# Optimization experiments

Measured on AMD Instinct MI355X. Metric: run time of the kernel, lower is better.

## Reference

```python
import jax, jax.numpy as jnp
import numpy as np

B, S, D, H, E, K = 4, 512, 512, 2048, 8, 2
LN_EPS = 1e-5

def _ln(x, g, b):
    m = jnp.mean(x, axis=-1, keepdims=True)
    v = jnp.var(x, axis=-1, keepdims=True)
    return (x - m) / jnp.sqrt(v + LN_EPS) * g + b

def setup_inputs() -> dict:
    key = jax.random.key(0)
    ks = jax.random.split(key, 8)
    s = 0.02
    return {
        "x": jax.random.normal(ks[0], (B, S, D), dtype=jnp.float32),
        "context": jax.random.normal(ks[1], (B, S, D), dtype=jnp.float32),
        "quality": jax.random.uniform(ks[2], (B, 1), dtype=jnp.float32),
        "rn_g": jnp.ones((D,), jnp.float32), "rn_b": jnp.zeros((D,), jnp.float32),
        "cn_g": jnp.ones((D,), jnp.float32), "cn_b": jnp.zeros((D,), jnp.float32),
        "ctx_W": jax.random.normal(ks[3], (D, D), dtype=jnp.float32) * s,
        "ctx_b": jnp.zeros((D,), jnp.float32),
        "qual_W": jax.random.normal(ks[4], (1, D), dtype=jnp.float32) * s,
        "qual_b": jnp.zeros((D,), jnp.float32),
        "rtr_W": jax.random.normal(ks[5], (D, E), dtype=jnp.float32) * s,
        "rtr_b": jnp.zeros((E,), jnp.float32),
        "temperature": jnp.asarray(1.0, jnp.float32),
        "W1": jax.random.normal(ks[6], (E, D, H), dtype=jnp.float32) * s,
        "b1": jnp.zeros((E, H), jnp.float32),
        "W2": jax.random.normal(ks[7], (E, H, D), dtype=jnp.float32) * s,
        "b2": jnp.zeros((E, D), jnp.float32),
    }

def reference(x, context, quality, rn_g, rn_b, cn_g, cn_b, ctx_W, ctx_b,
              qual_W, qual_b, rtr_W, rtr_b, temperature, W1, b1, W2, b2):
    # router features: LN(x) + context_proj(LN(context)) + quality_proj(quality)
    rf = _ln(x, rn_g, rn_b) + (_ln(context, cn_g, cn_b) @ ctx_W + ctx_b)
    q = quality[:, None, :]                      # [B,1,1]
    rf = rf + (q @ qual_W + qual_b)              # broadcast [B,1,D] over seq
    logits = (rf @ rtr_W + rtr_b) / jnp.maximum(temperature, 0.25)  # [B,S,E]
    # eval mode: no router noise, no dropout
    topk_logits, topk_idx = jax.lax.top_k(logits, K)
    gates = jax.nn.softmax(topk_logits, axis=-1)                    # [B,S,K]
    # per-token per-expert combine weight (equivalent to masked dispatch)
    combine = jnp.sum(gates[..., None] * jax.nn.one_hot(topk_idx, E, dtype=x.dtype), axis=-2)  # [B,S,E]
    # dense all-expert FFN, combined with (mostly zero) gate weights
    h = jax.nn.gelu(jnp.einsum('bsd,edh->bseh', x, W1) + b1, approximate=False)  # [B,S,E,H]
    y = jnp.einsum('bseh,ehd->bsed', h, W2) + b2                                 # [B,S,E,D]
    out = jnp.einsum('bsed,bse->bsd', y, combine)
    # aux losses
    probs = jax.nn.softmax(logits, axis=-1)
    importance = probs.mean(axis=(0, 1))
    load_balance = jnp.mean((importance - 1.0 / E) ** 2)
    router_z = jnp.mean(jax.scipy.special.logsumexp(logits, axis=-1) ** 2)
    entropy = jnp.mean(-jnp.sum(probs * jnp.log(jnp.clip(probs, 1e-9, None)), axis=-1))
    aux = load_balance + 1e-3 * router_z - 1e-3 * entropy
    return out, load_balance, router_z, entropy, aux
```

## Files before the change

kernel.cpp:

```cpp
#include <hip/hip_runtime.h>
#include <hip/hip_bf16.h>
#include <math.h>

#define Bb 4
#define Ss 512
#define Dd 512
#define Hh 2048
#define Ee 8
#define TOKENS 2048
#define CAP 2048

typedef __attribute__((ext_vector_type(8))) _Float16 f16x8;
typedef __attribute__((ext_vector_type(4))) _Float16 f16x4;
typedef __attribute__((ext_vector_type(4))) float f32x4;

#define WS_CNT   0
#define WS_OFFS  32
#define WS_M1    128
#define WS_QV    16512
#define WS_CB    16544
#define WS_LIST  16640
#define WS_GLIST 82176
#define WS_LOG   147712
#define WS_XF    (WS_LOG + 65536)
#define WS_W1F   (WS_XF + 2097152)
#define WS_W2F   (WS_W1F + 16777216)
#define WS_HF    (WS_W2F + 16777216)

__device__ __forceinline__ float wred(float v) {
#pragma unroll
  for (int o = 32; o > 0; o >>= 1) v += __shfl_down(v, o);
  return v;
}

__device__ __forceinline__ float wredx(float v) {
#pragma unroll
  for (int o = 32; o > 0; o >>= 1) v += __shfl_xor(v, o);
  return v;
}

__device__ __forceinline__ float block_sum(float v, float* s4, int tid) {
  v = wred(v);
  __syncthreads();
  if ((tid & 63) == 0) s4[tid >> 6] = v;
  __syncthreads();
  return s4[0] + s4[1] + s4[2] + s4[3];
}

__device__ __forceinline__ float gelu_f(float v) {
  return 0.5f * v * (1.0f + erff(v * 0.7071067811865475f));
}

#define GL16(gp, lp) __builtin_amdgcn_global_load_lds( \
    (const __attribute__((address_space(1))) void*)(gp), \
    (__attribute__((address_space(3))) void*)(lp), 16, 0, 0)

__global__ __launch_bounds__(64) void k_precomp(
    const float* __restrict__ ctx_W, const float* __restrict__ rtr_W,
    const float* __restrict__ rtr_b, const float* __restrict__ qual_W,
    const float* __restrict__ qual_b, const float* __restrict__ ctx_b,
    float* __restrict__ M1, float* __restrict__ qv, float* __restrict__ cb) {
  int d = blockIdx.x;
  int lane = threadIdx.x;
  if (d < Dd) {
    float acc[Ee] = {0.f, 0.f, 0.f, 0.f, 0.f, 0.f, 0.f, 0.f};
    for (int k = lane; k < Dd; k += 64) {
      float cw = ctx_W[d * Dd + k];
      const float* r = rtr_W + k * Ee;
#pragma unroll
      for (int e = 0; e < Ee; e++) acc[e] += cw * r[e];
    }
#pragma unroll
    for (int e = 0; e < Ee; e++) acc[e] = wred(acc[e]);
    if (lane == 0) {
#pragma unroll
      for (int e = 0; e < Ee; e++) M1[d * Ee + e] = acc[e];
    }
  } else {
    float aq[Ee] = {0.f, 0.f, 0.f, 0.f, 0.f, 0.f, 0.f, 0.f};
    float ab[Ee] = {0.f, 0.f, 0.f, 0.f, 0.f, 0.f, 0.f, 0.f};
    for (int k = lane; k < Dd; k += 64) {
      float qw = qual_W[k];
      float bb = ctx_b[k] + qual_b[k];
      const float* r = rtr_W + k * Ee;
#pragma unroll
      for (int e = 0; e < Ee; e++) {
        aq[e] += qw * r[e];
        ab[e] += bb * r[e];
      }
    }
#pragma unroll
    for (int e = 0; e < Ee; e++) {
      aq[e] = wred(aq[e]);
      ab[e] = wred(ab[e]);
    }
    if (lane == 0) {
#pragma unroll
      for (int e = 0; e < Ee; e++) {
        qv[e] = aq[e];
        cb[e] = ab[e] + rtr_b[e];
      }
    }
  }
}

__global__ __launch_bounds__(256) void k_logits(
    const float* __restrict__ x, const float* __restrict__ ctx,
    const float* __restrict__ quality, const float* __restrict__ rn_g,
    const float* __restrict__ rn_b, const float* __restrict__ cn_g,
    const float* __restrict__ cn_b, const float* __restrict__ rtr_W,
    const float* __restrict__ M1, const float* __restrict__ qv,
    const float* __restrict__ cb, const float* __restrict__ temperature,
    float* __restrict__ logitsS, _Float16* __restrict__ xf) {
  int wid = threadIdx.x >> 6, lane = threadIdx.x & 63;
  int t = blockIdx.x * 4 + wid;
  int d0 = lane * 8;

  float xv[8], cv[8];
  *(float4*)&xv[0] = *(const float4*)(x + (size_t)t * Dd + d0);
  *(float4*)&xv[4] = *(const float4*)(x + (size_t)t * Dd + d0 + 4);
  *(float4*)&cv[0] = *(const float4*)(ctx + (size_t)t * Dd + d0);
  *(float4*)&cv[4] = *(const float4*)(ctx + (size_t)t * Dd + d0 + 4);

  f16x8 xh;
#pragma unroll
  for (int d = 0; d < 8; d++) xh[d] = (_Float16)xv[d];
  *(f16x8*)(xf + (size_t)t * Dd + d0) = xh;

  float sx = 0.f, sc = 0.f;
#pragma unroll
  for (int d = 0; d < 8; d++) { sx += xv[d]; sc += cv[d]; }
  float mx = wredx(sx) * (1.f / Dd);
  float mc = wredx(sc) * (1.f / Dd);
  float vx = 0.f, vc = 0.f;
#pragma unroll
  for (int d = 0; d < 8; d++) {
    vx += (xv[d] - mx) * (xv[d] - mx);
    vc += (cv[d] - mc) * (cv[d] - mc);
  }
  float rsx = rsqrtf(wredx(vx) * (1.f / Dd) + 1e-5f);
  float rsc = rsqrtf(wredx(vc) * (1.f / Dd) + 1e-5f);

  float rg[8], rb[8], cg[8], cbb[8];
  *(float4*)&rg[0] = *(const float4*)(rn_g + d0);
  *(float4*)&rg[4] = *(const float4*)(rn_g + d0 + 4);
  *(float4*)&rb[0] = *(const float4*)(rn_b + d0);
  *(float4*)&rb[4] = *(const float4*)(rn_b + d0 + 4);
  *(float4*)&cg[0] = *(const float4*)(cn_g + d0);
  *(float4*)&cg[4] = *(const float4*)(cn_g + d0 + 4);
  *(float4*)&cbb[0] = *(const float4*)(cn_b + d0);
  *(float4*)&cbb[4] = *(const float4*)(cn_b + d0 + 4);

  float lg[Ee] = {0.f, 0.f, 0.f, 0.f, 0.f, 0.f, 0.f, 0.f};
#pragma unroll
  for (int d = 0; d < 8; d++) {
    float xn = (xv[d] - mx) * rsx * rg[d] + rb[d];
    float cn = (cv[d] - mc) * rsc * cg[d] + cbb[d];
    float rw[8], m1[8];
    *(float4*)&rw[0] = *(const float4*)(rtr_W + (size_t)(d0 + d) * Ee);
    *(float4*)&rw[4] = *(const float4*)(rtr_W + (size_t)(d0 + d) * Ee + 4);
    *(float4*)&m1[0] = *(const float4*)(M1 + (size_t)(d0 + d) * Ee);
    *(float4*)&m1[4] = *(const float4*)(M1 + (size_t)(d0 + d) * Ee + 4);
#pragma unroll
    for (int e = 0; e < Ee; e++) lg[e] += xn * rw[e] + cn * m1[e];
  }
#pragma unroll
  for (int e = 0; e < Ee; e++) lg[e] = wredx(lg[e]);

  if (lane == 0) {
    float invT = 1.f / fmaxf(temperature[0], 0.25f);
    float q = quality[t / Ss];
    float L[8];
#pragma unroll
    for (int e = 0; e < Ee; e++) L[e] = (lg[e] + q * qv[e] + cb[e]) * invT;
    *(float4*)(logitsS + (size_t)t * Ee) = *(float4*)&L[0];
    *(float4*)(logitsS + (size_t)t * Ee + 4) = *(float4*)&L[4];
  }
}

__global__ __launch_bounds__(256) void k_select(
    const float* __restrict__ logitsS, int* __restrict__ cnt,
    int* __restrict__ offs, int* __restrict__ list,
    float* __restrict__ glist, float* __restrict__ out) {
  __shared__ int scnt[Ee];
  __shared__ float s4[4];
  int tid = threadIdx.x;
  if (tid < Ee) scnt[tid] = 0;
  __syncthreads();

  float impL[Ee] = {0.f, 0.f, 0.f, 0.f, 0.f, 0.f, 0.f, 0.f};
  float zL = 0.f, eL = 0.f;

#pragma unroll
  for (int j = 0; j < 8; j++) {
    int t = j * 256 + tid;
    float L[8];
    *(float4*)&L[0] = *(const float4*)(logitsS + (size_t)t * Ee);
    *(float4*)&L[4] = *(const float4*)(logitsS + (size_t)t * Ee + 4);

    int i0 = 0;
#pragma unroll
    for (int e = 1; e < Ee; e++)
      if (L[e] > L[i0]) i0 = e;
    int i1 = (i0 == 0) ? 1 : 0;
#pragma unroll
    for (int e = 0; e < Ee; e++)
      if (e != i0 && L[e] > L[i1]) i1 = e;

    float e1 = __expf(L[i1] - L[i0]);
    float g0 = 1.f / (1.f + e1);
    float g1 = e1 / (1.f + e1);

    float m = L[i0];
    float p[8];
    float sum = 0.f;
#pragma unroll
    for (int e = 0; e < Ee; e++) {
      p[e] = __expf(L[e] - m);
      sum += p[e];
    }
    float lse = m + __logf(sum);
    float inv = 1.f / sum;
    zL += lse * lse;
#pragma unroll
    for (int e = 0; e < Ee; e++) {
      p[e] *= inv;
      eL -= p[e] * __logf(fmaxf(p[e], 1e-9f));
      impL[e] += p[e];
    }

    int s0 = atomicAdd(&scnt[i0], 1);
    list[i0 * CAP + s0] = t;
    glist[i0 * CAP + s0] = g0;
    int s1 = atomicAdd(&scnt[i1], 1);
    list[i1 * CAP + s1] = t;
    glist[i1 * CAP + s1] = g1;
  }

  float impS[Ee];
#pragma unroll
  for (int e = 0; e < Ee; e++) impS[e] = block_sum(impL[e], s4, tid);
  float zS = block_sum(zL, s4, tid);
  float eS = block_sum(eL, s4, tid);
  __syncthreads();

  if (tid == 0) {
    int s = 0;
#pragma unroll
    for (int e = 0; e < Ee; e++) {
      cnt[e] = scnt[e];
      offs[e] = s;
      s += scnt[e];
    }
    float lb = 0.f;
#pragma unroll
    for (int e = 0; e < Ee; e++) {
      float v = impS[e] * (1.f / TOKENS) - (1.f / Ee);
      lb += v * v;
    }
    lb *= (1.f / Ee);
    float rz = zS * (1.f / TOKENS);
    float en = eS * (1.f / TOKENS);
    float* sp = out + (size_t)Bb * Ss * Dd;
    sp[0] = lb;
    sp[1] = rz;
    sp[2] = en;
    sp[3] = lb + 0.001f * rz - 0.001f * en;
  }
}

__device__ __forceinline__ void convT_tile(const float* __restrict__ src,
    _Float16* __restrict__ dst, int R, int C, int bx, float* ls) {
  int nr = R >> 6, ncc = C >> 6;
  int e = bx / (nr * ncc);
  int rem = bx % (nr * ncc);
  int rt = rem / ncc, ct = rem % ncc;
  int tid = threadIdx.x;
  const float* s0 = src + (size_t)e * R * C + (size_t)(rt * 64) * C + ct * 64;
#pragma unroll
  for (int j = 0; j < 4; j++) {
    int li = j * 256 + tid;
    int rr = li >> 4, c4 = (li & 15) << 2;
    float4 v = *(const float4*)(s0 + (size_t)rr * C + c4);
    ls[rr * 65 + c4] = v.x;
    ls[rr * 65 + c4 + 1] = v.y;
    ls[rr * 65 + c4 + 2] = v.z;
    ls[rr * 65 + c4 + 3] = v.w;
  }
  __syncthreads();
#pragma unroll
  for (int j = 0; j < 4; j++) {
    int li = j * 256 + tid;
    int on = li >> 4, k4 = (li & 15) << 2;
    f16x4 o;
    o[0] = (_Float16)ls[(k4 + 0) * 65 + on];
    o[1] = (_Float16)ls[(k4 + 1) * 65 + on];
    o[2] = (_Float16)ls[(k4 + 2) * 65 + on];
    o[3] = (_Float16)ls[(k4 + 3) * 65 + on];
    *(f16x4*)(dst + ((size_t)e * C + ct * 64 + on) * R + rt * 64 + k4) = o;
  }
}

__global__ __launch_bounds__(256) void k_convW(
    const float* __restrict__ W1, const float* __restrict__ W2,
    _Float16* __restrict__ w1f, _Float16* __restrict__ w2f) {
  __shared__ float ls[64 * 65];
  int bx = blockIdx.x;
  if (bx < Ee * 8 * 32) {
    convT_tile(W1, w1f, Dd, Hh, bx, ls);
  } else {
    convT_tile(W2, w2f, Hh, Dd, bx - Ee * 8 * 32, ls);
  }
}

__global__ __launch_bounds__(256) void k_mg1(
    const _Float16* __restrict__ xf, const _Float16* __restrict__ w1f,
    const float* __restrict__ b1,
    const int* __restrict__ cnt, const int* __restrict__ offs,
    const int* __restrict__ list, _Float16* __restrict__ hf) {
  int bx = blockIdx.x;
  int e = bx >> 9;
  int r = (bx >> 4) & 31;
  int c = bx & 15;
  int ne = cnt[e];
  if (r * 64 >= ne) return;
  int off = offs[e];

  __shared__ _Float16 As[2][4 * 64 * 8];
  __shared__ _Float16 Bs[2][4 * 128 * 8];
  __shared__ int stok[64];

  int tid = threadIdx.x;
  if (tid < 64) {
    int row = r * 64 + tid;
    stok[tid] = list[e * CAP + ((row < ne) ? row : (ne - 1))];
  }
  __syncthreads();

  int ag = tid >> 6, arow = tid & 63;
  size_t asrc = (size_t)stok[arow] * Dd + ag * 8;
  int bg0 = tid >> 7, brow0 = tid & 127;
  size_t bsrc0 = ((size_t)(e * Hh + c * 128 + brow0)) * Dd + bg0 * 8;
  size_t bsrc1 = bsrc0 + 16;
  int aL = (ag * 64 + arow) * 8;
  int bL0 = (bg0 * 128 + brow0) * 8;
  int bL1 = ((bg0 + 2) * 128 + brow0) * 8;

  int lane = tid & 63, wid = tid >> 6;
  int wm = wid >> 1, wn = wid & 1;
  int l15 = lane & 15, lg = lane >> 4;

  f32x4 acc[2][4] = {};

  GL16(xf + asrc, &As[0][aL]);
  GL16(w1f + bsrc0, &Bs[0][bL0]);
  GL16(w1f + bsrc1, &Bs[0][bL1]);
  __syncthreads();

  int cur = 0;
  for (int k0 = 32; k0 <= Dd; k0 += 32) {
    if (k0 < Dd) {
      GL16(xf + asrc + k0, &As[cur ^ 1][aL]);
      GL16(w1f + bsrc0 + k0, &Bs[cur ^ 1][bL0]);
      GL16(w1f + bsrc1 + k0, &Bs[cur ^ 1][bL1]);
    }
    f16x8 a[2], b[4];
#pragma unroll
    for (int m = 0; m < 2; m++)
      a[m] = *(const f16x8*)&As[cur][(lg * 64 + wm * 32 + m * 16 + l15) * 8];
#pragma unroll
    for (int n = 0; n < 4; n++)
      b[n] = *(const f16x8*)&Bs[cur][(lg * 128 + wn * 64 + n * 16 + l15) * 8];
#pragma unroll
    for (int m = 0; m < 2; m++)
#pragma unroll
      for (int n = 0; n < 4; n++)
        acc[m][n] = __builtin_amdgcn_mfma_f32_16x16x32_f16(a[m], b[n], acc[m][n], 0, 0, 0);
    __syncthreads();
    cur ^= 1;
  }

  int lg4 = lg * 4;
#pragma unroll
  for (int n = 0; n < 4; n++) {
    int colg = c * 128 + wn * 64 + n * 16 + l15;
    float bias = b1[e * Hh + colg];
#pragma unroll
    for (int m = 0; m < 2; m++) {
#pragma unroll
      for (int j = 0; j < 4; j++) {
        int rowl = r * 64 + wm * 32 + m * 16 + lg4 + j;
        if (rowl < ne)
          hf[(size_t)(off + rowl) * Hh + colg] = (_Float16)gelu_f(acc[m][n][j] + bias);
      }
    }
  }
}

__global__ __launch_bounds__(256) void k_mg2(
    const _Float16* __restrict__ hf, const _Float16* __restrict__ w2f,
    const float* __restrict__ b2,
    const int* __restrict__ cnt, const int* __restrict__ offs,
    const int* __restrict__ list, const float* __restrict__ glist,
    float* __restrict__ out) {
  int bx = blockIdx.x;
  int e = bx >> 8;
  int r = (bx >> 3) & 31;
  int c = (bx >> 1) & 3;
  int kS = bx & 1;
  int ne = cnt[e];
  if (r * 64 >= ne) return;
  int off = offs[e];

  __shared__ _Float16 As[2][4 * 64 * 8];
  __shared__ _Float16 Bs[2][4 * 128 * 8];

  int tid = threadIdx.x;
  int ag = tid >> 6, arow = tid & 63;
  int ar = r * 64 + arow;
  if (ar >= ne) ar = ne - 1;
  size_t kb = (size_t)kS * 1024;
  size_t asrc = (size_t)(off + ar) * Hh + kb + ag * 8;
  int bg0 = tid >> 7, brow0 = tid & 127;
  size_t bsrc0 = ((size_t)(e * Dd + c * 128 + brow0)) * Hh + kb + bg0 * 8;
  size_t bsrc1 = bsrc0 + 16;
  int aL = (ag * 64 + arow) * 8;
  int bL0 = (bg0 * 128 + brow0) * 8;
  int bL1 = ((bg0 + 2) * 128 + brow0) * 8;

  int lane = tid & 63, wid = tid >> 6;
  int wm = wid >> 1, wn = wid & 1;
  int l15 = lane & 15, lg = lane >> 4;

  f32x4 acc[2][4] = {};

  GL16(hf + asrc, &As[0][aL]);
  GL16(w2f + bsrc0, &Bs[0][bL0]);
  GL16(w2f + bsrc1, &Bs[0][bL1]);
  __syncthreads();

  int cur = 0;
  for (int k0 = 32; k0 <= 1024; k0 += 32) {
    if (k0 < 1024) {
      GL16(hf + asrc + k0, &As[cur ^ 1][aL]);
      GL16(w2f + bsrc0 + k0, &Bs[cur ^ 1][bL0]);
      GL16(w2f + bsrc1 + k0, &Bs[cur ^ 1][bL1]);
    }
    f16x8 a[2], b[4];
#pragma unroll
    for (int m = 0; m < 2; m++)
      a[m] = *(const f16x8*)&As[cur][(lg * 64 + wm * 32 + m * 16 + l15) * 8];
#pragma unroll
    for (int n = 0; n < 4; n++)
      b[n] = *(const f16x8*)&Bs[cur][(lg * 128 + wn * 64 + n * 16 + l15) * 8];
#pragma unroll
    for (int m = 0; m < 2; m++)
#pragma unroll
      for (int n = 0; n < 4; n++)
        acc[m][n] = __builtin_amdgcn_mfma_f32_16x16x32_f16(a[m], b[n], acc[m][n], 0, 0, 0);
    __syncthreads();
    cur ^= 1;
  }

  int lg4 = lg * 4;
#pragma unroll
  for (int m = 0; m < 2; m++) {
#pragma unroll
    for (int j = 0; j < 4; j++) {
      int rowl = r * 64 + wm * 32 + m * 16 + lg4 + j;
      if (rowl < ne) {
        int tok = list[e * CAP + rowl];
        float gte = glist[e * CAP + rowl];
#pragma unroll
        for (int n = 0; n < 4; n++) {
          int colg = c * 128 + wn * 64 + n * 16 + l15;
          float v = acc[m][n][j] + (kS == 0 ? b2[e * Dd + colg] : 0.f);
          atomicAdd(&out[(size_t)tok * Dd + colg], gte * v);
        }
      }
    }
  }
}

extern "C" void kernel_launch(void* const* d_in, const int* in_sizes, int n_in,
                              void* d_out, int out_size, void* d_ws, size_t ws_size,
                              hipStream_t stream) {
  const float* x = (const float*)d_in[0];
  const float* ctx = (const float*)d_in[1];
  const float* quality = (const float*)d_in[2];
  const float* rn_g = (const float*)d_in[3];
  const float* rn_b = (const float*)d_in[4];
  const float* cn_g = (const float*)d_in[5];
  const float* cn_b = (const float*)d_in[6];
  const float* ctx_W = (const float*)d_in[7];
  const float* ctx_b = (const float*)d_in[8];
  const float* qual_W = (const float*)d_in[9];
  const float* qual_b = (const float*)d_in[10];
  const float* rtr_W = (const float*)d_in[11];
  const float* rtr_b = (const float*)d_in[12];
  const float* temperature = (const float*)d_in[13];
  const float* W1 = (const float*)d_in[14];
  const float* b1 = (const float*)d_in[15];
  const float* W2 = (const float*)d_in[16];
  const float* b2 = (const float*)d_in[17];
  float* out = (float*)d_out;

  char* w = (char*)d_ws;
  int* cnt = (int*)(w + WS_CNT);
  int* offs = (int*)(w + WS_OFFS);
  float* M1 = (float*)(w + WS_M1);
  float* qv = (float*)(w + WS_QV);
  float* cb = (float*)(w + WS_CB);
  int* list = (int*)(w + WS_LIST);
  float* glist = (float*)(w + WS_GLIST);
  float* logitsS = (float*)(w + WS_LOG);
  _Float16* xf = (_Float16*)(w + WS_XF);
  _Float16* w1f = (_Float16*)(w + WS_W1F);
  _Float16* w2f = (_Float16*)(w + WS_W2F);
  _Float16* hf = (_Float16*)(w + WS_HF);

  hipMemsetAsync(d_out, 0, (size_t)out_size * sizeof(float), stream);

  k_precomp<<<513, 64, 0, stream>>>(ctx_W, rtr_W, rtr_b, qual_W, qual_b, ctx_b, M1, qv, cb);
  k_logits<<<TOKENS / 4, 256, 0, stream>>>(x, ctx, quality, rn_g, rn_b, cn_g, cn_b, rtr_W,
                                           M1, qv, cb, temperature, logitsS, xf);
  k_convW<<<Ee * 8 * 32 * 2, 256, 0, stream>>>(W1, W2, w1f, w2f);
  k_select<<<1, 256, 0, stream>>>(logitsS, cnt, offs, list, glist, out);
  k_mg1<<<Ee * 32 * 16, 256, 0, stream>>>(xf, w1f, b1, cnt, offs, list, hf);
  k_mg2<<<Ee * 32 * 4 * 2, 256, 0, stream>>>(hf, w2f, b2, cnt, offs, list, glist, out);
}
```

Before: 297.7 us.

## Enlarge grouped GEMM tiles to 128x128, widen K step, fuse weight conversion launch

```diff
diff --git a/kernel.cpp b/kernel.cpp
--- a/kernel.cpp
+++ b/kernel.cpp
@@ -55,13 +55,57 @@
     (const __attribute__((address_space(1))) void*)(gp), \
     (__attribute__((address_space(3))) void*)(lp), 16, 0, 0)
 
-__global__ __launch_bounds__(64) void k_precomp(
+__device__ __forceinline__ void convT_tile(const float* __restrict__ src,
+    _Float16* __restrict__ dst, int R, int C, int bx, float* ls) {
+  int nr = R >> 6, ncc = C >> 6;
+  int e = bx / (nr * ncc);
+  int rem = bx % (nr * ncc);
+  int rt = rem / ncc, ct = rem % ncc;
+  int tid = threadIdx.x;
+  const float* s0 = src + (size_t)e * R * C + (size_t)(rt * 64) * C + ct * 64;
+#pragma unroll
+  for (int j = 0; j < 4; j++) {
+    int li = j * 256 + tid;
+    int rr = li >> 4, c4 = (li & 15) << 2;
+    float4 v = *(const float4*)(s0 + (size_t)rr * C + c4);
+    ls[rr * 65 + c4] = v.x;
+    ls[rr * 65 + c4 + 1] = v.y;
+    ls[rr * 65 + c4 + 2] = v.z;
+    ls[rr * 65 + c4 + 3] = v.w;
+  }
+  __syncthreads();
+#pragma unroll
+  for (int j = 0; j < 4; j++) {
+    int li = j * 256 + tid;
+    int on = li >> 4, k4 = (li & 15) << 2;
+    f16x4 o;
+    o[0] = (_Float16)ls[(k4 + 0) * 65 + on];
+    o[1] = (_Float16)ls[(k4 + 1) * 65 + on];
+    o[2] = (_Float16)ls[(k4 + 2) * 65 + on];
+    o[3] = (_Float16)ls[(k4 + 3) * 65 + on];
+    *(f16x4*)(dst + ((size_t)e * C + ct * 64 + on) * R + rt * 64 + k4) = o;
+  }
+}
+
+__global__ __launch_bounds__(256) void k_pre(
     const float* __restrict__ ctx_W, const float* __restrict__ rtr_W,
     const float* __restrict__ rtr_b, const float* __restrict__ qual_W,
     const float* __restrict__ qual_b, const float* __restrict__ ctx_b,
-    float* __restrict__ M1, float* __restrict__ qv, float* __restrict__ cb) {
-  int d = blockIdx.x;
-  int lane = threadIdx.x;
+    const float* __restrict__ W1, const float* __restrict__ W2,
+    float* __restrict__ M1, float* __restrict__ qv, float* __restrict__ cb,
+    _Float16* __restrict__ w1f, _Float16* __restrict__ w2f) {
+  __shared__ float ls[64 * 65];
+  int bx = blockIdx.x;
+  if (bx >= 513) {
+    int cx = bx - 513;
+    if (cx < Ee * 8 * 32) convT_tile(W1, w1f, Dd, Hh, cx, ls);
+    else convT_tile(W2, w2f, Hh, Dd, cx - Ee * 8 * 32, ls);
+    return;
+  }
+  int d = bx;
+  int tid = threadIdx.x;
+  if (tid >= 64) return;
+  int lane = tid;
   if (d < Dd) {
     float acc[Ee] = {0.f, 0.f, 0.f, 0.f, 0.f, 0.f, 0.f, 0.f};
     for (int k = lane; k < Dd; k += 64) {
@@ -269,115 +313,72 @@
   }
 }
 
-__device__ __forceinline__ void convT_tile(const float* __restrict__ src,
-    _Float16* __restrict__ dst, int R, int C, int bx, float* ls) {
-  int nr = R >> 6, ncc = C >> 6;
-  int e = bx / (nr * ncc);
-  int rem = bx % (nr * ncc);
-  int rt = rem / ncc, ct = rem % ncc;
-  int tid = threadIdx.x;
-  const float* s0 = src + (size_t)e * R * C + (size_t)(rt * 64) * C + ct * 64;
-#pragma unroll
-  for (int j = 0; j < 4; j++) {
-    int li = j * 256 + tid;
-    int rr = li >> 4, c4 = (li & 15) << 2;
-    float4 v = *(const float4*)(s0 + (size_t)rr * C + c4);
-    ls[rr * 65 + c4] = v.x;
-    ls[rr * 65 + c4 + 1] = v.y;
-    ls[rr * 65 + c4 + 2] = v.z;
-    ls[rr * 65 + c4 + 3] = v.w;
-  }
-  __syncthreads();
-#pragma unroll
-  for (int j = 0; j < 4; j++) {
-    int li = j * 256 + tid;
-    int on = li >> 4, k4 = (li & 15) << 2;
-    f16x4 o;
-    o[0] = (_Float16)ls[(k4 + 0) * 65 + on];
-    o[1] = (_Float16)ls[(k4 + 1) * 65 + on];
-    o[2] = (_Float16)ls[(k4 + 2) * 65 + on];
-    o[3] = (_Float16)ls[(k4 + 3) * 65 + on];
-    *(f16x4*)(dst + ((size_t)e * C + ct * 64 + on) * R + rt * 64 + k4) = o;
-  }
-}
-
-__global__ __launch_bounds__(256) void k_convW(
-    const float* __restrict__ W1, const float* __restrict__ W2,
-    _Float16* __restrict__ w1f, _Float16* __restrict__ w2f) {
-  __shared__ float ls[64 * 65];
-  int bx = blockIdx.x;
-  if (bx < Ee * 8 * 32) {
-    convT_tile(W1, w1f, Dd, Hh, bx, ls);
-  } else {
-    convT_tile(W2, w2f, Hh, Dd, bx - Ee * 8 * 32, ls);
-  }
-}
-
 __global__ __launch_bounds__(256) void k_mg1(
     const _Float16* __restrict__ xf, const _Float16* __restrict__ w1f,
     const float* __restrict__ b1,
     const int* __restrict__ cnt, const int* __restrict__ offs,
     const int* __restrict__ list, _Float16* __restrict__ hf) {
   int bx = blockIdx.x;
-  int e = bx >> 9;
-  int r = (bx >> 4) & 31;
+  int e = bx >> 8;
+  int r = (bx >> 4) & 15;
   int c = bx & 15;
   int ne = cnt[e];
-  if (r * 64 >= ne) return;
+  if (r * 128 >= ne) return;
   int off = offs[e];
 
-  __shared__ _Float16 As[2][4 * 64 * 8];
-  __shared__ _Float16 Bs[2][4 * 128 * 8];
-  __shared__ int stok[64];
+  __shared__ _Float16 As[8 * 128 * 8];
+  __shared__ _Float16 Bs[8 * 128 * 8];
+  __shared__ int stok[128];
 
   int tid = threadIdx.x;
-  if (tid < 64) {
-    int row = r * 64 + tid;
+  if (tid < 128) {
+    int row = r * 128 + tid;
     stok[tid] = list[e * CAP + ((row < ne) ? row : (ne - 1))];
   }
   __syncthreads();
 
-  int ag = tid >> 6, arow = tid & 63;
-  size_t asrc = (size_t)stok[arow] * Dd + ag * 8;
-  int bg0 = tid >> 7, brow0 = tid & 127;
-  size_t bsrc0 = ((size_t)(e * Hh + c * 128 + brow0)) * Dd + bg0 * 8;
-  size_t bsrc1 = bsrc0 + 16;
-  int aL = (ag * 64 + arow) * 8;
-  int bL0 = (bg0 * 128 + brow0) * 8;
-  int bL1 = ((bg0 + 2) * 128 + brow0) * 8;
+  size_t asrc[4], bsrc[4];
+  int lq[4];
+#pragma unroll
+  for (int q = 0; q < 4; q++) {
+    int idx = q * 256 + tid;
+    int g = idx >> 7, row = idx & 127;
+    asrc[q] = (size_t)stok[row] * Dd + g * 8;
+    bsrc[q] = ((size_t)(e * Hh + c * 128 + row)) * Dd + g * 8;
+    lq[q] = idx * 8;
+  }
 
   int lane = tid & 63, wid = tid >> 6;
   int wm = wid >> 1, wn = wid & 1;
   int l15 = lane & 15, lg = lane >> 4;
 
-  f32x4 acc[2][4] = {};
-
-  GL16(xf + asrc, &As[0][aL]);
-  GL16(w1f + bsrc0, &Bs[0][bL0]);
-  GL16(w1f + bsrc1, &Bs[0][bL1]);
-  __syncthreads();
-
-  int cur = 0;
-  for (int k0 = 32; k0 <= Dd; k0 += 32) {
-    if (k0 < Dd) {
-      GL16(xf + asrc + k0, &As[cur ^ 1][aL]);
-      GL16(w1f + bsrc0 + k0, &Bs[cur ^ 1][bL0]);
-      GL16(w1f + bsrc1 + k0, &Bs[cur ^ 1][bL1]);
-    }
-    f16x8 a[2], b[4];
-#pragma unroll
-    for (int m = 0; m < 2; m++)
-      a[m] = *(const f16x8*)&As[cur][(lg * 64 + wm * 32 + m * 16 + l15) * 8];
-#pragma unroll
-    for (int n = 0; n < 4; n++)
-      b[n] = *(const f16x8*)&Bs[cur][(lg * 128 + wn * 64 + n * 16 + l15) * 8];
-#pragma unroll
-    for (int m = 0; m < 2; m++)
+  f32x4 acc[4][4] = {};
+
+  for (int k0 = 0; k0 < Dd; k0 += 64) {
+#pragma unroll
+    for (int q = 0; q < 4; q++) {
+      GL16(xf + asrc[q] + k0, &As[lq[q]]);
+      GL16(w1f + bsrc[q] + k0, &Bs[lq[q]]);
+    }
+    __syncthreads();
+    f16x8 a[2][4], b[2][4];
+#pragma unroll
+    for (int ks = 0; ks < 2; ks++) {
+#pragma unroll
+      for (int m = 0; m < 4; m++)
+        a[ks][m] = *(const f16x8*)&As[(((ks * 4 + lg) << 7) + wm * 64 + m * 16 + l15) * 8];
 #pragma unroll
       for (int n = 0; n < 4; n++)
-        acc[m][n] = __builtin_amdgcn_mfma_f32_16x16x32_f16(a[m], b[n], acc[m][n], 0, 0, 0);
+        b[ks][n] = *(const f16x8*)&Bs[(((ks * 4 + lg) << 7) + wn * 64 + n * 16 + l15) * 8];
+    }
+#pragma unroll
+    for (int ks = 0; ks < 2; ks++)
+#pragma unroll
+      for (int m = 0; m < 4; m++)
+#pragma unroll
+        for (int n = 0; n < 4; n++)
+          acc[m][n] = __builtin_amdgcn_mfma_f32_16x16x32_f16(a[ks][m], b[ks][n], acc[m][n], 0, 0, 0);
     __syncthreads();
-    cur ^= 1;
   }
 
   int lg4 = lg * 4;
@@ -386,10 +387,10 @@
     int colg = c * 128 + wn * 64 + n * 16 + l15;
     float bias = b1[e * Hh + colg];
 #pragma unroll
-    for (int m = 0; m < 2; m++) {
+    for (int m = 0; m < 4; m++) {
 #pragma unroll
       for (int j = 0; j < 4; j++) {
-        int rowl = r * 64 + wm * 32 + m * 16 + lg4 + j;
+        int rowl = r * 128 + wm * 64 + m * 16 + lg4 + j;
         if (rowl < ne)
           hf[(size_t)(off + rowl) * Hh + colg] = (_Float16)gelu_f(acc[m][n][j] + bias);
       }
@@ -405,69 +406,71 @@
     float* __restrict__ out) {
   int bx = blockIdx.x;
   int e = bx >> 8;
-  int r = (bx >> 3) & 31;
-  int c = (bx >> 1) & 3;
-  int kS = bx & 1;
+  int r = (bx >> 4) & 15;
+  int c = (bx >> 2) & 3;
+  int kS = bx & 3;
   int ne = cnt[e];
-  if (r * 64 >= ne) return;
+  if (r * 128 >= ne) return;
   int off = offs[e];
 
-  __shared__ _Float16 As[2][4 * 64 * 8];
-  __shared__ _Float16 Bs[2][4 * 128 * 8];
+  __shared__ _Float16 As[8 * 128 * 8];
+  __shared__ _Float16 Bs[8 * 128 * 8];
 
   int tid = threadIdx.x;
-  int ag = tid >> 6, arow = tid & 63;
-  int ar = r * 64 + arow;
-  if (ar >= ne) ar = ne - 1;
-  size_t kb = (size_t)kS * 1024;
-  size_t asrc = (size_t)(off + ar) * Hh + kb + ag * 8;
-  int bg0 = tid >> 7, brow0 = tid & 127;
-  size_t bsrc0 = ((size_t)(e * Dd + c * 128 + brow0)) * Hh + kb + bg0 * 8;
-  size_t bsrc1 = bsrc0 + 16;
-  int aL = (ag * 64 + arow) * 8;
-  int bL0 = (bg0 * 128 + brow0) * 8;
-  int bL1 = ((bg0 + 2) * 128 + brow0) * 8;
+  size_t kbase = (size_t)kS * 512;
+
+  size_t asrc[4], bsrc[4];
+  int lq[4];
+#pragma unroll
+  for (int q = 0; q < 4; q++) {
+    int idx = q * 256 + tid;
+    int g = idx >> 7, row = idx & 127;
+    int ar = r * 128 + row;
+    if (ar >= ne) ar = ne - 1;
+    asrc[q] = (size_t)(off + ar) * Hh + kbase + g * 8;
+    bsrc[q] = ((size_t)(e * Dd + c * 128 + row)) * Hh + kbase + g * 8;
+    lq[q] = idx * 8;
+  }
 
   int lane = tid & 63, wid = tid >> 6;
   int wm = wid >> 1, wn = wid & 1;
   int l15 = lane & 15, lg = lane >> 4;
 
-  f32x4 acc[2][4] = {};
-
-  GL16(hf + asrc, &As[0][aL]);
-  GL16(w2f + bsrc0, &Bs[0][bL0]);
-  GL16(w2f + bsrc1, &Bs[0][bL1]);
-  __syncthreads();
-
-  int cur = 0;
-  for (int k0 = 32; k0 <= 1024; k0 += 32) {
-    if (k0 < 1024) {
-      GL16(hf + asrc + k0, &As[cur ^ 1][aL]);
-      GL16(w2f + bsrc0 + k0, &Bs[cur ^ 1][bL0]);
-      GL16(w2f + bsrc1 + k0, &Bs[cur ^ 1][bL1]);
-    }
-    f16x8 a[2], b[4];
-#pragma unroll
-    for (int m = 0; m < 2; m++)
-      a[m] = *(const f16x8*)&As[cur][(lg * 64 + wm * 32 + m * 16 + l15) * 8];
-#pragma unroll
-    for (int n = 0; n < 4; n++)
-      b[n] = *(const f16x8*)&Bs[cur][(lg * 128 + wn * 64 + n * 16 + l15) * 8];
-#pragma unroll
-    for (int m = 0; m < 2; m++)
+  f32x4 acc[4][4] = {};
+
+  for (int k0 = 0; k0 < 512; k0 += 64) {
+#pragma unroll
+    for (int q = 0; q < 4; q++) {
+      GL16(hf + asrc[q] + k0, &As[lq[q]]);
+      GL16(w2f + bsrc[q] + k0, &Bs[lq[q]]);
+    }
+    __syncthreads();
+    f16x8 a[2][4], b[2][4];
+#pragma unroll
+    for (int ks = 0; ks < 2; ks++) {
+#pragma unroll
+      for (int m = 0; m < 4; m++)
+        a[ks][m] = *(const f16x8*)&As[(((ks * 4 + lg) << 7) + wm * 64 + m * 16 + l15) * 8];
 #pragma unroll
       for (int n = 0; n < 4; n++)
-        acc[m][n] = __builtin_amdgcn_mfma_f32_16x16x32_f16(a[m], b[n], acc[m][n], 0, 0, 0);
+        b[ks][n] = *(const f16x8*)&Bs[(((ks * 4 + lg) << 7) + wn * 64 + n * 16 + l15) * 8];
+    }
+#pragma unroll
+    for (int ks = 0; ks < 2; ks++)
+#pragma unroll
+      for (int m = 0; m < 4; m++)
+#pragma unroll
+        for (int n = 0; n < 4; n++)
+          acc[m][n] = __builtin_amdgcn_mfma_f32_16x16x32_f16(a[ks][m], b[ks][n], acc[m][n], 0, 0, 0);
     __syncthreads();
-    cur ^= 1;
   }
 
   int lg4 = lg * 4;
 #pragma unroll
-  for (int m = 0; m < 2; m++) {
+  for (int m = 0; m < 4; m++) {
 #pragma unroll
     for (int j = 0; j < 4; j++) {
-      int rowl = r * 64 + wm * 32 + m * 16 + lg4 + j;
+      int rowl = r * 128 + wm * 64 + m * 16 + lg4 + j;
       if (rowl < ne) {
         int tok = list[e * CAP + rowl];
         float gte = glist[e * CAP + rowl];
@@ -521,11 +524,11 @@
 
   hipMemsetAsync(d_out, 0, (size_t)out_size * sizeof(float), stream);
 
-  k_precomp<<<513, 64, 0, stream>>>(ctx_W, rtr_W, rtr_b, qual_W, qual_b, ctx_b, M1, qv, cb);
+  k_pre<<<513 + Ee * 8 * 32 * 2, 256, 0, stream>>>(
+      ctx_W, rtr_W, rtr_b, qual_W, qual_b, ctx_b, W1, W2, M1, qv, cb, w1f, w2f);
   k_logits<<<TOKENS / 4, 256, 0, stream>>>(x, ctx, quality, rn_g, rn_b, cn_g, cn_b, rtr_W,
                                            M1, qv, cb, temperature, logitsS, xf);
-  k_convW<<<Ee * 8 * 32 * 2, 256, 0, stream>>>(W1, W2, w1f, w2f);
   k_select<<<1, 256, 0, stream>>>(logitsS, cnt, offs, list, glist, out);
-  k_mg1<<<Ee * 32 * 16, 256, 0, stream>>>(xf, w1f, b1, cnt, offs, list, hf);
-  k_mg2<<<Ee * 32 * 4 * 2, 256, 0, stream>>>(hf, w2f, b2, cnt, offs, list, glist, out);
-}
+  k_mg1<<<Ee * 16 * 16, 256, 0, stream>>>(xf, w1f, b1, cnt, offs, list, hf);
+  k_mg2<<<Ee * 16 * 4 * 4, 256, 0, stream>>>(hf, w2f, b2, cnt, offs, list, glist, out);
+}
```

New measurement: 271.9 us. 8.7% less time.
